# Kernel tuning notes

Measured on AMD Instinct MI355X. Metric: run time of the kernel, lower is better.

Reference implementation:

```python
import jax, jax.numpy as jnp
import numpy as np

N_NODES = 50000
N_EDGES = 800000
D = 64
NUM_GRAPHS = 64


def gcn_conv(x, src, dst, deg_inv_sqrt, W, b):
    # GCNConv: h = X W; out_i = sum_{j->i} norm_ij * h_j + self-loop term + b
    h = x @ W  # [N, D_out]
    norm = deg_inv_sqrt[src] * deg_inv_sqrt[dst]  # [E]
    msgs = h[src] * norm[:, None]  # [E, D_out] -- dominant gather
    out = jax.ops.segment_sum(msgs, dst, num_segments=N_NODES)
    # self-loop edge (i,i) with norm = deg_i^-1
    out = out + h * (deg_inv_sqrt ** 2)[:, None]
    return out + b


def setup_inputs() -> dict:
    key = jax.random.key(0)
    ks = jax.random.split(key, 12)
    x = jax.random.normal(ks[0], (N_NODES, D), dtype=jnp.float32)
    edge_index = jax.random.randint(ks[1], (2, N_EDGES), 0, N_NODES, dtype=jnp.int64)
    batch = jnp.sort(jax.random.randint(ks[2], (N_NODES,), 0, NUM_GRAPHS, dtype=jnp.int64))
    s = 1.0 / np.sqrt(D)
    W1 = jax.random.uniform(ks[3], (D, D), jnp.float32, -s, s)
    b1 = jnp.zeros((D,), jnp.float32)
    W2 = jax.random.uniform(ks[4], (D, D), jnp.float32, -s, s)
    b2 = jnp.zeros((D,), jnp.float32)
    W3 = jax.random.uniform(ks[5], (D, D), jnp.float32, -s, s)
    b3 = jnp.zeros((D,), jnp.float32)
    Wl = jax.random.uniform(ks[6], (D, 1), jnp.float32, -s, s)
    bl = jnp.zeros((1,), jnp.float32)
    return {"x": x, "edge_index": edge_index, "batch": batch,
            "W1": W1, "b1": b1, "W2": W2, "b2": b2, "W3": W3, "b3": b3,
            "Wl": Wl, "bl": bl}


def reference(x, edge_index, batch, W1, b1, W2, b2, W3, b3, Wl, bl):
    src, dst = edge_index[0], edge_index[1]
    # symmetric GCN normalization with self-loops: deg_i = in_degree_i + 1
    deg = jax.ops.segment_sum(jnp.ones((N_EDGES,), x.dtype), dst, num_segments=N_NODES) + 1.0
    deg_inv_sqrt = deg ** -0.5
    h = jax.nn.relu(gcn_conv(x, src, dst, deg_inv_sqrt, W1, b1))
    h = jax.nn.relu(gcn_conv(h, src, dst, deg_inv_sqrt, W2, b2))
    h = jax.nn.relu(gcn_conv(h, src, dst, deg_inv_sqrt, W3, b3))
    # global mean pool over graphs
    sums = jax.ops.segment_sum(h, batch, num_segments=NUM_GRAPHS)  # [G, D]
    counts = jax.ops.segment_sum(jnp.ones((N_NODES,), h.dtype), batch, num_segments=NUM_GRAPHS)
    pooled = sums / jnp.clip(counts, 1.0)[:, None]
    return pooled @ Wl + bl  # [G, 1]
```

## Files before the change

### kernel.cpp

```cpp
#include <hip/hip_runtime.h>

#define N_NODES 50000
#define N_EDGES 800000
#define DIM 64
#define NUM_GRAPHS 64

__global__ void count_deg_kernel(const int* __restrict__ dst, int* __restrict__ cnt, int E) {
  int e = blockIdx.x * blockDim.x + threadIdx.x;
  if (e < E) atomicAdd(&cnt[dst[e]], 1);
}

__global__ void scanA_kernel(const int* __restrict__ cnt, int* __restrict__ rowptr,
                             int* __restrict__ bsum, float* __restrict__ dis, int N) {
  __shared__ int wsum[16];
  int i = blockIdx.x * 1024 + threadIdx.x;
  int lane = threadIdx.x & 63, wid = threadIdx.x >> 6;
  int v = (i < N) ? cnt[i] : 0;
  if (i < N) dis[i] = rsqrtf((float)(v + 1));
  int sv = v;
  #pragma unroll
  for (int off = 1; off < 64; off <<= 1) {
    int t = __shfl_up(sv, off, 64);
    if (lane >= off) sv += t;
  }
  if (lane == 63) wsum[wid] = sv;
  __syncthreads();
  if (wid == 0) {
    int wv = (lane < 16) ? wsum[lane] : 0;
    #pragma unroll
    for (int off = 1; off < 16; off <<= 1) {
      int t = __shfl_up(wv, off, 64);
      if (lane >= off) wv += t;
    }
    if (lane < 16) wsum[lane] = wv;
  }
  __syncthreads();
  if (i < N) rowptr[i] = (wid ? wsum[wid - 1] : 0) + (sv - v);
  if (threadIdx.x == 1023) bsum[blockIdx.x] = wsum[15];
}

__global__ void scanB_kernel(int* __restrict__ bsum, int* __restrict__ rowptr, int nb, int N) {
  int t = threadIdx.x;
  int v = (t < nb) ? bsum[t] : 0;
  #pragma unroll
  for (int off = 1; off < 64; off <<= 1) {
    int u = __shfl_up(v, off, 64);
    if (t >= off) v += u;
  }
  if (t < nb) bsum[t] = v;
  if (t == nb - 1) rowptr[N] = v;
}

__global__ void scanC_kernel(int* __restrict__ rowptr, const int* __restrict__ bsum,
                             int* __restrict__ cursor, int N) {
  int b = blockIdx.x;
  int i = b * 1024 + threadIdx.x;
  if (i < N) {
    int off = b ? bsum[b - 1] : 0;
    int r = rowptr[i] + off;
    rowptr[i] = r;
    cursor[i] = r;
  }
}

__global__ void fill_kernel(const int* __restrict__ src, const int* __restrict__ dst,
                            int* __restrict__ cursor, int* __restrict__ esrc, int E) {
  int e = blockIdx.x * blockDim.x + threadIdx.x;
  if (e < E) {
    int d = dst[e];
    int p = atomicAdd(&cursor[d], 1);
    esrc[p] = src[e];
  }
}

__global__ __launch_bounds__(256) void aggregate_kernel(const float* __restrict__ F,
    const int* __restrict__ rowptr, const int* __restrict__ esrc,
    const float* __restrict__ dis, float* __restrict__ A, int N) {
  int node = blockIdx.x * 4 + (threadIdx.x >> 6);
  if (node >= N) return;
  int lane = threadIdx.x & 63;
  int qc = lane & 15;
  int qe = lane >> 4;
  const float4* __restrict__ F4 = reinterpret_cast<const float4*>(F);
  int beg = rowptr[node], end = rowptr[node + 1];
  float ax = 0.f, ay = 0.f, az = 0.f, aw = 0.f;
  int j = beg;
  for (; j + 8 <= end; j += 8) {
    int s0 = esrc[j + qe], s1 = esrc[j + 4 + qe];
    float d0 = dis[s0], d1 = dis[s1];
    float4 v0 = F4[(size_t)s0 * 16 + qc];
    float4 v1 = F4[(size_t)s1 * 16 + qc];
    ax = fmaf(v0.x, d0, ax); ay = fmaf(v0.y, d0, ay);
    az = fmaf(v0.z, d0, az); aw = fmaf(v0.w, d0, aw);
    ax = fmaf(v1.x, d1, ax); ay = fmaf(v1.y, d1, ay);
    az = fmaf(v1.z, d1, az); aw = fmaf(v1.w, d1, aw);
  }
  if (j + 4 <= end) {
    int s0 = esrc[j + qe];
    float d0 = dis[s0];
    float4 v0 = F4[(size_t)s0 * 16 + qc];
    ax = fmaf(v0.x, d0, ax); ay = fmaf(v0.y, d0, ay);
    az = fmaf(v0.z, d0, az); aw = fmaf(v0.w, d0, aw);
    j += 4;
  }
  if (j + qe < end) {
    int s = esrc[j + qe];
    float d = dis[s];
    float4 v = F4[(size_t)s * 16 + qc];
    ax = fmaf(v.x, d, ax); ay = fmaf(v.y, d, ay);
    az = fmaf(v.z, d, az); aw = fmaf(v.w, d, aw);
  }
  ax += __shfl_xor(ax, 16, 64); ax += __shfl_xor(ax, 32, 64);
  ay += __shfl_xor(ay, 16, 64); ay += __shfl_xor(ay, 32, 64);
  az += __shfl_xor(az, 16, 64); az += __shfl_xor(az, 32, 64);
  aw += __shfl_xor(aw, 16, 64); aw += __shfl_xor(aw, 32, 64);
  if (qe == 0) {
    float dn = dis[node];
    float4 sf = F4[(size_t)node * 16 + qc];
    float4 r;
    r.x = (ax + sf.x * dn) * dn;
    r.y = (ay + sf.y * dn) * dn;
    r.z = (az + sf.z * dn) * dn;
    r.w = (aw + sf.w * dn) * dn;
    reinterpret_cast<float4*>(A)[(size_t)node * 16 + qc] = r;
  }
}

__global__ __launch_bounds__(256) void gemm_bias_relu(const float* __restrict__ X,
    const float* __restrict__ W, const float* __restrict__ b,
    float* __restrict__ F, int N) {
  __shared__ float4 Xs[64][16];
  int col = threadIdx.x & 63, wid = threadIdx.x >> 6;
  float wreg[DIM];
  #pragma unroll
  for (int k = 0; k < DIM; ++k) wreg[k] = W[k * DIM + col];
  float bias = b[col];
  int row0 = blockIdx.x * 64;
  for (int i = threadIdx.x; i < 64 * 16; i += 256) {
    int r = i >> 4, c = i & 15;
    int gr = row0 + r;
    Xs[r][c] = (gr < N) ? reinterpret_cast<const float4*>(X)[(size_t)gr * 16 + c]
                        : make_float4(0.f, 0.f, 0.f, 0.f);
  }
  __syncthreads();
  for (int rr = 0; rr < 16; ++rr) {
    int lr = wid * 16 + rr;
    int row = row0 + lr;
    if (row >= N) break;
    float a0 = 0.f, a1 = 0.f, a2 = 0.f, a3 = 0.f;
    #pragma unroll
    for (int kk = 0; kk < 16; ++kk) {
      float4 xv = Xs[lr][kk];
      a0 = fmaf(xv.x, wreg[4 * kk + 0], a0);
      a1 = fmaf(xv.y, wreg[4 * kk + 1], a1);
      a2 = fmaf(xv.z, wreg[4 * kk + 2], a2);
      a3 = fmaf(xv.w, wreg[4 * kk + 3], a3);
    }
    float v = a0 + a1 + a2 + a3 + bias;
    F[(size_t)row * DIM + col] = fmaxf(v, 0.f);
  }
}

__global__ __launch_bounds__(256) void gemm_dot_kernel(const float* __restrict__ X,
    const float* __restrict__ W, const float* __restrict__ b, const float* __restrict__ Wl,
    const int* __restrict__ batch, float* __restrict__ partial, int N) {
  __shared__ float4 Xs[64][16];
  __shared__ float yv[64];
  __shared__ float gpart[NUM_GRAPHS];
  int col = threadIdx.x & 63, wid = threadIdx.x >> 6;
  float wreg[DIM];
  #pragma unroll
  for (int k = 0; k < DIM; ++k) wreg[k] = W[k * DIM + col];
  float bias = b[col];
  float wl = Wl[col];
  int row0 = blockIdx.x * 64;
  if (threadIdx.x < 64) { yv[threadIdx.x] = 0.f; gpart[threadIdx.x] = 0.f; }
  for (int i = threadIdx.x; i < 64 * 16; i += 256) {
    int r = i >> 4, c = i & 15;
    int gr = row0 + r;
    Xs[r][c] = (gr < N) ? reinterpret_cast<const float4*>(X)[(size_t)gr * 16 + c]
                        : make_float4(0.f, 0.f, 0.f, 0.f);
  }
  __syncthreads();
  for (int rr = 0; rr < 16; ++rr) {
    int lr = wid * 16 + rr;
    int row = row0 + lr;
    if (row >= N) break;
    float a0 = 0.f, a1 = 0.f, a2 = 0.f, a3 = 0.f;
    #pragma unroll
    for (int kk = 0; kk < 16; ++kk) {
      float4 xv = Xs[lr][kk];
      a0 = fmaf(xv.x, wreg[4 * kk + 0], a0);
      a1 = fmaf(xv.y, wreg[4 * kk + 1], a1);
      a2 = fmaf(xv.z, wreg[4 * kk + 2], a2);
      a3 = fmaf(xv.w, wreg[4 * kk + 3], a3);
    }
    float v = fmaxf(a0 + a1 + a2 + a3 + bias, 0.f);
    float y = v * wl;
    #pragma unroll
    for (int off = 32; off > 0; off >>= 1) y += __shfl_down(y, off, 64);
    if (col == 0) yv[lr] = y;
  }
  __syncthreads();
  if (threadIdx.x < 64) {
    int row = row0 + threadIdx.x;
    if (row < N) atomicAdd(&gpart[batch[row]], yv[threadIdx.x]);
  }
  __syncthreads();
  if (threadIdx.x < NUM_GRAPHS) {
    int glo = batch[row0];
    int ghi = batch[min(row0 + 63, N - 1)];
    int g = threadIdx.x;
    if (g >= glo && g <= ghi) atomicAdd(&partial[g], gpart[g]);
  }
}

__global__ void pool_final_kernel(const float* __restrict__ partial, const int* __restrict__ batch,
                                  const float* __restrict__ bl, float* __restrict__ out, int N) {
  int g = threadIdx.x;
  int lo = 0, hi = N;
  while (lo < hi) { int m = (lo + hi) >> 1; if (batch[m] < g) lo = m + 1; else hi = m; }
  int start = lo;
  hi = N;
  while (lo < hi) { int m = (lo + hi) >> 1; if (batch[m] < g + 1) lo = m + 1; else hi = m; }
  float c = fmaxf((float)(lo - start), 1.f);
  out[g] = partial[g] / c + bl[0];
}

extern "C" void kernel_launch(void* const* d_in, const int* in_sizes, int n_in,
                              void* d_out, int out_size, void* d_ws, size_t ws_size,
                              hipStream_t stream) {
  const float* x     = (const float*)d_in[0];
  const int*   ei    = (const int*)d_in[1];
  const int*   batch = (const int*)d_in[2];
  const float* W1 = (const float*)d_in[3];
  const float* b1 = (const float*)d_in[4];
  const float* W2 = (const float*)d_in[5];
  const float* b2 = (const float*)d_in[6];
  const float* W3 = (const float*)d_in[7];
  const float* b3 = (const float*)d_in[8];
  const float* Wl = (const float*)d_in[9];
  const float* bl = (const float*)d_in[10];
  float* out = (float*)d_out;

  const int* srcp = ei;
  const int* dstp = ei + N_EDGES;

  char* ws = (char*)d_ws;
  size_t off = 0;
  auto alloc = [&](size_t bytes) { void* p = ws + off; off += (bytes + 255) & ~(size_t)255; return p; };
  int*   cnt     = (int*)  alloc((size_t)N_NODES * 4);
  float* dis     = (float*)alloc((size_t)N_NODES * 4);
  int*   rowptr  = (int*)  alloc((size_t)(N_NODES + 1) * 4);
  int*   bsum    = (int*)  alloc(64 * 4);
  float* partial = (float*)alloc(NUM_GRAPHS * 4);
  int*   esrc    = (int*)  alloc((size_t)N_EDGES * 4);
  float* bufA    = (float*)alloc((size_t)N_NODES * DIM * 4);
  float* bufB    = (float*)alloc((size_t)N_NODES * DIM * 4);

  const int NB = (N_NODES + 1023) / 1024;

  hipMemsetAsync(cnt, 0, (size_t)N_NODES * 4, stream);
  count_deg_kernel<<<(N_EDGES + 255) / 256, 256, 0, stream>>>(dstp, cnt, N_EDGES);
  scanA_kernel<<<NB, 1024, 0, stream>>>(cnt, rowptr, bsum, dis, N_NODES);
  scanB_kernel<<<1, 64, 0, stream>>>(bsum, rowptr, NB, N_NODES);
  scanC_kernel<<<NB, 1024, 0, stream>>>(rowptr, bsum, cnt, N_NODES);
  fill_kernel<<<(N_EDGES + 255) / 256, 256, 0, stream>>>(srcp, dstp, cnt, esrc, N_EDGES);

  const int GB = (N_NODES + 63) / 64;
  aggregate_kernel<<<(N_NODES + 3) / 4, 256, 0, stream>>>(x, rowptr, esrc, dis, bufA, N_NODES);
  gemm_bias_relu<<<GB, 256, 0, stream>>>(bufA, W1, b1, bufB, N_NODES);
  aggregate_kernel<<<(N_NODES + 3) / 4, 256, 0, stream>>>(bufB, rowptr, esrc, dis, bufA, N_NODES);
  gemm_bias_relu<<<GB, 256, 0, stream>>>(bufA, W2, b2, bufB, N_NODES);
  aggregate_kernel<<<(N_NODES + 3) / 4, 256, 0, stream>>>(bufB, rowptr, esrc, dis, bufA, N_NODES);
  hipMemsetAsync(partial, 0, NUM_GRAPHS * 4, stream);
  gemm_dot_kernel<<<GB, 256, 0, stream>>>(bufA, W3, b3, Wl, batch, partial, N_NODES);
  pool_final_kernel<<<1, 64, 0, stream>>>(partial, batch, bl, out, N_NODES);
}
```

Measured before the change: 260.9 us.

## Fuse aggregation and dense GEMM into one persistent per-layer kernel

Merges each layer's neighbour aggregation with the following 64x64 matmul, bias and ReLU into a single persistent kernel. Each wave aggregates one node and then broadcasts the aggregated row through readlane to compute the GEMM from register-held weights. This removes the intermediate buffer round-trip and three kernel launches. The last layer does the Wl dot product with one global atomic per node. The risks are serialised readlane/FMA chains per node, heavy register pressure from wreg, and more global atomics on the 64 partial sums.

```diff
diff --git a/kernel.cpp b/kernel.cpp
--- a/kernel.cpp
+++ b/kernel.cpp
@@ -73,145 +73,90 @@
   }
 }
 
-__global__ __launch_bounds__(256) void aggregate_kernel(const float* __restrict__ F,
+__device__ __forceinline__ float rl(float v, int lane) {
+  return __int_as_float(__builtin_amdgcn_readlane(__float_as_int(v), lane));
+}
+
+template <int LAST>
+__global__ __launch_bounds__(256) void fused_layer(const float* __restrict__ F,
     const int* __restrict__ rowptr, const int* __restrict__ esrc,
-    const float* __restrict__ dis, float* __restrict__ A, int N) {
-  int node = blockIdx.x * 4 + (threadIdx.x >> 6);
-  if (node >= N) return;
-  int lane = threadIdx.x & 63;
-  int qc = lane & 15;
-  int qe = lane >> 4;
-  const float4* __restrict__ F4 = reinterpret_cast<const float4*>(F);
-  int beg = rowptr[node], end = rowptr[node + 1];
-  float ax = 0.f, ay = 0.f, az = 0.f, aw = 0.f;
-  int j = beg;
-  for (; j + 8 <= end; j += 8) {
-    int s0 = esrc[j + qe], s1 = esrc[j + 4 + qe];
-    float d0 = dis[s0], d1 = dis[s1];
-    float4 v0 = F4[(size_t)s0 * 16 + qc];
-    float4 v1 = F4[(size_t)s1 * 16 + qc];
-    ax = fmaf(v0.x, d0, ax); ay = fmaf(v0.y, d0, ay);
-    az = fmaf(v0.z, d0, az); aw = fmaf(v0.w, d0, aw);
-    ax = fmaf(v1.x, d1, ax); ay = fmaf(v1.y, d1, ay);
-    az = fmaf(v1.z, d1, az); aw = fmaf(v1.w, d1, aw);
-  }
-  if (j + 4 <= end) {
-    int s0 = esrc[j + qe];
-    float d0 = dis[s0];
-    float4 v0 = F4[(size_t)s0 * 16 + qc];
-    ax = fmaf(v0.x, d0, ax); ay = fmaf(v0.y, d0, ay);
-    az = fmaf(v0.z, d0, az); aw = fmaf(v0.w, d0, aw);
-    j += 4;
-  }
-  if (j + qe < end) {
-    int s = esrc[j + qe];
-    float d = dis[s];
-    float4 v = F4[(size_t)s * 16 + qc];
-    ax = fmaf(v.x, d, ax); ay = fmaf(v.y, d, ay);
-    az = fmaf(v.z, d, az); aw = fmaf(v.w, d, aw);
-  }
-  ax += __shfl_xor(ax, 16, 64); ax += __shfl_xor(ax, 32, 64);
-  ay += __shfl_xor(ay, 16, 64); ay += __shfl_xor(ay, 32, 64);
-  az += __shfl_xor(az, 16, 64); az += __shfl_xor(az, 32, 64);
-  aw += __shfl_xor(aw, 16, 64); aw += __shfl_xor(aw, 32, 64);
-  if (qe == 0) {
-    float dn = dis[node];
-    float4 sf = F4[(size_t)node * 16 + qc];
-    float4 r;
-    r.x = (ax + sf.x * dn) * dn;
-    r.y = (ay + sf.y * dn) * dn;
-    r.z = (az + sf.z * dn) * dn;
-    r.w = (aw + sf.w * dn) * dn;
-    reinterpret_cast<float4*>(A)[(size_t)node * 16 + qc] = r;
-  }
-}
-
-__global__ __launch_bounds__(256) void gemm_bias_relu(const float* __restrict__ X,
-    const float* __restrict__ W, const float* __restrict__ b,
-    float* __restrict__ F, int N) {
-  __shared__ float4 Xs[64][16];
-  int col = threadIdx.x & 63, wid = threadIdx.x >> 6;
+    const float* __restrict__ dis, const float* __restrict__ W,
+    const float* __restrict__ b, float* __restrict__ Fout,
+    const float* __restrict__ Wl, const int* __restrict__ batch,
+    float* __restrict__ partial, int N) {
+  int col = threadIdx.x & 63;
+  int wid = threadIdx.x >> 6;
+  int wave = blockIdx.x * 4 + wid;
+  int nwaves = gridDim.x * 4;
+  int qc = col & 15;
+  int qe = col >> 4;
+
   float wreg[DIM];
   #pragma unroll
   for (int k = 0; k < DIM; ++k) wreg[k] = W[k * DIM + col];
   float bias = b[col];
-  int row0 = blockIdx.x * 64;
-  for (int i = threadIdx.x; i < 64 * 16; i += 256) {
-    int r = i >> 4, c = i & 15;
-    int gr = row0 + r;
-    Xs[r][c] = (gr < N) ? reinterpret_cast<const float4*>(X)[(size_t)gr * 16 + c]
-                        : make_float4(0.f, 0.f, 0.f, 0.f);
-  }
-  __syncthreads();
-  for (int rr = 0; rr < 16; ++rr) {
-    int lr = wid * 16 + rr;
-    int row = row0 + lr;
-    if (row >= N) break;
-    float a0 = 0.f, a1 = 0.f, a2 = 0.f, a3 = 0.f;
+  float wl = LAST ? Wl[col] : 0.f;
+
+  const float4* __restrict__ F4 = reinterpret_cast<const float4*>(F);
+
+  for (int node = wave; node < N; node += nwaves) {
+    int beg = rowptr[node], end = rowptr[node + 1];
+    float ax = 0.f, ay = 0.f, az = 0.f, aw = 0.f;
+    int j = beg;
+    for (; j + 8 <= end; j += 8) {
+      int s0 = esrc[j + qe], s1 = esrc[j + 4 + qe];
+      float d0 = dis[s0], d1 = dis[s1];
+      float4 v0 = F4[(size_t)s0 * 16 + qc];
+      float4 v1 = F4[(size_t)s1 * 16 + qc];
+      ax = fmaf(v0.x, d0, ax); ay = fmaf(v0.y, d0, ay);
+      az = fmaf(v0.z, d0, az); aw = fmaf(v0.w, d0, aw);
+      ax = fmaf(v1.x, d1, ax); ay = fmaf(v1.y, d1, ay);
+      az = fmaf(v1.z, d1, az); aw = fmaf(v1.w, d1, aw);
+    }
+    if (j + 4 <= end) {
+      int s0 = esrc[j + qe];
+      float d0 = dis[s0];
+      float4 v0 = F4[(size_t)s0 * 16 + qc];
+      ax = fmaf(v0.x, d0, ax); ay = fmaf(v0.y, d0, ay);
+      az = fmaf(v0.z, d0, az); aw = fmaf(v0.w, d0, aw);
+      j += 4;
+    }
+    if (j + qe < end) {
+      int s = esrc[j + qe];
+      float d = dis[s];
+      float4 v = F4[(size_t)s * 16 + qc];
+      ax = fmaf(v.x, d, ax); ay = fmaf(v.y, d, ay);
+      az = fmaf(v.z, d, az); aw = fmaf(v.w, d, aw);
+    }
+    ax += __shfl_xor(ax, 16, 64); ax += __shfl_xor(ax, 32, 64);
+    ay += __shfl_xor(ay, 16, 64); ay += __shfl_xor(ay, 32, 64);
+    az += __shfl_xor(az, 16, 64); az += __shfl_xor(az, 32, 64);
+    aw += __shfl_xor(aw, 16, 64); aw += __shfl_xor(aw, 32, 64);
+
+    float dn = dis[node];
+    float4 sf = F4[(size_t)node * 16 + qc];
+    float rx = (ax + sf.x * dn) * dn;
+    float ry = (ay + sf.y * dn) * dn;
+    float rz = (az + sf.z * dn) * dn;
+    float rw = (aw + sf.w * dn) * dn;
+
+    float acc = bias;
     #pragma unroll
-    for (int kk = 0; kk < 16; ++kk) {
-      float4 xv = Xs[lr][kk];
-      a0 = fmaf(xv.x, wreg[4 * kk + 0], a0);
-      a1 = fmaf(xv.y, wreg[4 * kk + 1], a1);
-      a2 = fmaf(xv.z, wreg[4 * kk + 2], a2);
-      a3 = fmaf(xv.w, wreg[4 * kk + 3], a3);
-    }
-    float v = a0 + a1 + a2 + a3 + bias;
-    F[(size_t)row * DIM + col] = fmaxf(v, 0.f);
-  }
-}
-
-__global__ __launch_bounds__(256) void gemm_dot_kernel(const float* __restrict__ X,
-    const float* __restrict__ W, const float* __restrict__ b, const float* __restrict__ Wl,
-    const int* __restrict__ batch, float* __restrict__ partial, int N) {
-  __shared__ float4 Xs[64][16];
-  __shared__ float yv[64];
-  __shared__ float gpart[NUM_GRAPHS];
-  int col = threadIdx.x & 63, wid = threadIdx.x >> 6;
-  float wreg[DIM];
-  #pragma unroll
-  for (int k = 0; k < DIM; ++k) wreg[k] = W[k * DIM + col];
-  float bias = b[col];
-  float wl = Wl[col];
-  int row0 = blockIdx.x * 64;
-  if (threadIdx.x < 64) { yv[threadIdx.x] = 0.f; gpart[threadIdx.x] = 0.f; }
-  for (int i = threadIdx.x; i < 64 * 16; i += 256) {
-    int r = i >> 4, c = i & 15;
-    int gr = row0 + r;
-    Xs[r][c] = (gr < N) ? reinterpret_cast<const float4*>(X)[(size_t)gr * 16 + c]
-                        : make_float4(0.f, 0.f, 0.f, 0.f);
-  }
-  __syncthreads();
-  for (int rr = 0; rr < 16; ++rr) {
-    int lr = wid * 16 + rr;
-    int row = row0 + lr;
-    if (row >= N) break;
-    float a0 = 0.f, a1 = 0.f, a2 = 0.f, a3 = 0.f;
-    #pragma unroll
-    for (int kk = 0; kk < 16; ++kk) {
-      float4 xv = Xs[lr][kk];
-      a0 = fmaf(xv.x, wreg[4 * kk + 0], a0);
-      a1 = fmaf(xv.y, wreg[4 * kk + 1], a1);
-      a2 = fmaf(xv.z, wreg[4 * kk + 2], a2);
-      a3 = fmaf(xv.w, wreg[4 * kk + 3], a3);
-    }
-    float v = fmaxf(a0 + a1 + a2 + a3 + bias, 0.f);
-    float y = v * wl;
-    #pragma unroll
-    for (int off = 32; off > 0; off >>= 1) y += __shfl_down(y, off, 64);
-    if (col == 0) yv[lr] = y;
-  }
-  __syncthreads();
-  if (threadIdx.x < 64) {
-    int row = row0 + threadIdx.x;
-    if (row < N) atomicAdd(&gpart[batch[row]], yv[threadIdx.x]);
-  }
-  __syncthreads();
-  if (threadIdx.x < NUM_GRAPHS) {
-    int glo = batch[row0];
-    int ghi = batch[min(row0 + 63, N - 1)];
-    int g = threadIdx.x;
-    if (g >= glo && g <= ghi) atomicAdd(&partial[g], gpart[g]);
+    for (int c = 0; c < 16; ++c) {
+      acc = fmaf(rl(rx, c), wreg[4 * c + 0], acc);
+      acc = fmaf(rl(ry, c), wreg[4 * c + 1], acc);
+      acc = fmaf(rl(rz, c), wreg[4 * c + 2], acc);
+      acc = fmaf(rl(rw, c), wreg[4 * c + 3], acc);
+    }
+    float v = fmaxf(acc, 0.f);
+    if (!LAST) {
+      Fout[(size_t)node * DIM + col] = v;
+    } else {
+      float y = v * wl;
+      #pragma unroll
+      for (int off = 32; off > 0; off >>= 1) y += __shfl_xor(y, off, 64);
+      if (col == 0) atomicAdd(&partial[batch[node]], y);
+    }
   }
 }
 
@@ -267,13 +212,13 @@
   scanC_kernel<<<NB, 1024, 0, stream>>>(rowptr, bsum, cnt, N_NODES);
   fill_kernel<<<(N_EDGES + 255) / 256, 256, 0, stream>>>(srcp, dstp, cnt, esrc, N_EDGES);
 
-  const int GB = (N_NODES + 63) / 64;
-  aggregate_kernel<<<(N_NODES + 3) / 4, 256, 0, stream>>>(x, rowptr, esrc, dis, bufA, N_NODES);
-  gemm_bias_relu<<<GB, 256, 0, stream>>>(bufA, W1, b1, bufB, N_NODES);
-  aggregate_kernel<<<(N_NODES + 3) / 4, 256, 0, stream>>>(bufB, rowptr, esrc, dis, bufA, N_NODES);
-  gemm_bias_relu<<<GB, 256, 0, stream>>>(bufA, W2, b2, bufB, N_NODES);
-  aggregate_kernel<<<(N_NODES + 3) / 4, 256, 0, stream>>>(bufB, rowptr, esrc, dis, bufA, N_NODES);
+  const int FB = 2048;
+  fused_layer<0><<<FB, 256, 0, stream>>>(x,    rowptr, esrc, dis, W1, b1, bufA,
+                                         nullptr, nullptr, nullptr, N_NODES);
+  fused_layer<0><<<FB, 256, 0, stream>>>(bufA, rowptr, esrc, dis, W2, b2, bufB,
+                                         nullptr, nullptr, nullptr, N_NODES);
   hipMemsetAsync(partial, 0, NUM_GRAPHS * 4, stream);
-  gemm_dot_kernel<<<GB, 256, 0, stream>>>(bufA, W3, b3, Wl, batch, partial, N_NODES);
+  fused_layer<1><<<FB, 256, 0, stream>>>(bufB, rowptr, esrc, dis, W3, b3, nullptr,
+                                         Wl, batch, partial, N_NODES);
   pool_final_kernel<<<1, 64, 0, stream>>>(partial, batch, bl, out, N_NODES);
 }
```

Measured after the change: 592.3 us. 127% more time.
